# Performance work log

Hardware: AMD Instinct MI355X
Metric: run time of the kernel (lower is better)

## Reference

```python
import jax, jax.numpy as jnp
import numpy as np

NTYPES = 2
NATOMS = (512, 512)
N = 1024          # total atoms
NN = 128          # neighbors per type
M = NTYPES * NN   # 256 neighbor slots per atom
D = 25            # last embedding width
FH = 240          # fitting hidden width
B = 8
RMIN, RMAX = 5.8, 6.0


def _embed_mlp(s, W0, b0, W1, b1, W2, b2):
    # DeepMD-style resnet embedding net: 1 -> D -> D -> D, tanh + skip
    h = jnp.tanh(s @ W0 + b0)
    h = h + jnp.tanh(h @ W1 + b1)
    h = h + jnp.tanh(h @ W2 + b2)
    return h


def setup_inputs() -> dict:
    key = jax.random.key(0)
    ks = jax.random.split(key, 20)
    # relative positions; components in [-4.5, 4.5] so |r| spans <5.8, [5.8,6.0), >=6.0
    image_dR = (jax.random.uniform(ks[0], (B, N, NTYPES, NN, 3), jnp.float32) - 0.5) * 9.0
    # 0 == empty neighbor slot (mask = list_neigh > 0); index-1 in [0, N)
    list_neigh = jax.random.randint(ks[1], (B, N, NTYPES, NN), 0, 1025)
    davg = 0.1 * jax.random.normal(ks[2], (NTYPES, M, 4), jnp.float32)
    dstd = jax.random.uniform(ks[3], (NTYPES, M, 4), jnp.float32, 0.5, 1.5)
    P = NTYPES * NTYPES
    eW0 = jax.random.normal(ks[4], (P, 1, D), jnp.float32)
    eb0 = 0.1 * jax.random.normal(ks[5], (P, D), jnp.float32)
    eW1 = jax.random.normal(ks[6], (P, D, D), jnp.float32) / np.sqrt(D)
    eb1 = 0.1 * jax.random.normal(ks[7], (P, D), jnp.float32)
    eW2 = jax.random.normal(ks[8], (P, D, D), jnp.float32) / np.sqrt(D)
    eb2 = 0.1 * jax.random.normal(ks[9], (P, D), jnp.float32)
    fW0 = jax.random.normal(ks[10], (NTYPES, 16 * D, FH), jnp.float32) / np.sqrt(16 * D)
    fb0 = 0.1 * jax.random.normal(ks[11], (NTYPES, FH), jnp.float32)
    fW1 = jax.random.normal(ks[12], (NTYPES, FH, FH), jnp.float32) / np.sqrt(FH)
    fb1 = 0.1 * jax.random.normal(ks[13], (NTYPES, FH), jnp.float32)
    fW2 = jax.random.normal(ks[14], (NTYPES, FH, FH), jnp.float32) / np.sqrt(FH)
    fb2 = 0.1 * jax.random.normal(ks[15], (NTYPES, FH), jnp.float32)
    fW3 = jax.random.normal(ks[16], (NTYPES, FH, 1), jnp.float32) / np.sqrt(FH)
    fb3 = 0.1 * jax.random.normal(ks[17], (NTYPES, 1), jnp.float32)
    ener_shift = 0.01 * jax.random.normal(ks[18], (NTYPES,), jnp.float32)
    return {
        'image_dR': image_dR, 'list_neigh': list_neigh,
        'davg': davg, 'dstd': dstd,
        'eW0': eW0, 'eb0': eb0, 'eW1': eW1, 'eb1': eb1, 'eW2': eW2, 'eb2': eb2,
        'fW0': fW0, 'fb0': fb0, 'fW1': fW1, 'fb1': fb1, 'fW2': fW2, 'fb2': fb2,
        'fW3': fW3, 'fb3': fb3, 'ener_shift': ener_shift,
        'dfeat': jnp.zeros((1,), jnp.float32),
        'Egroup_weight': jnp.zeros((1,), jnp.float32),
        'divider': jnp.ones((1,), jnp.float32),
    }


def _forward(image_dR, list_neigh, davg, dstd,
             eW0, eb0, eW1, eb1, eW2, eb2,
             fW0, fb0, fW1, fb1, fW2, fb2, fW3, fb3, ener_shift):
    dR = image_dR.reshape(B, N, M, 3)
    neigh = list_neigh.reshape(B, N, M)
    mask = neigh > 0
    mf = mask.astype(dR.dtype)
    dR2 = jnp.sum(dR * dR, axis=-1)                       # [B,N,M]
    safe_dR2 = jnp.where(mask, dR2, 1.0)
    Rij = jnp.sqrt(safe_dR2)
    inr = mf / Rij                                        # 1/|r|, 0 off-mask
    x = Rij * mf                                          # nr = dR2/Rij = |r|
    Ri_xyz = dR / safe_dR2[..., None] * mf[..., None]     # r / |r|^2
    inr2 = inr * inr
    inr4 = inr2 * inr2
    inr3 = inr4 * x
    # smooth switching function on [RMIN, RMAX]
    u = (x - RMIN) / (RMAX - RMIN)
    poly = u * u * u * (-6.0 * u * u + 15.0 * u - 10.0) + 1.0
    dpoly = (3.0 * u * u * (-6.0 * u * u + 15.0 * u - 10.0)
             + u * u * u * (-12.0 * u + 15.0)) / (RMAX - RMIN)
    mid = (x >= RMIN) & (x < RMAX)
    vv = jnp.where(x < RMIN, 1.0, jnp.where(mid, poly, 0.0)) * mf
    dvv = jnp.where(mid, dpoly, 0.0) * mf
    Ri_pre = jnp.concatenate([inr[..., None], Ri_xyz], axis=-1)   # [B,N,M,4]
    common = (dvv * inr)[..., None] * dR                          # [B,N,M,3]
    row0 = dR * (inr3 * vv)[..., None] - Ri_pre[..., 0:1] * common
    eye = jnp.eye(3, dtype=dR.dtype)
    outer = (2.0 * dR[..., :, None] * dR[..., None, :] * inr4[..., None, None]
             - eye * inr2[..., None, None])                       # [B,N,M,3,3]
    rows = outer * vv[..., None, None] - Ri_pre[..., 1:4, None] * common[..., None, :]
    Ri_d = jnp.concatenate([row0[..., None, :], rows], axis=-2) * mf[..., None, None]  # [B,N,M,4,3]
    Ri = Ri_pre * vv[..., None]
    # per-type normalization stats broadcast over atoms of each type
    davg_res = jnp.concatenate([jnp.broadcast_to(davg[t], (NATOMS[t], M, 4)) for t in range(NTYPES)], axis=0)
    dstd_res = jnp.concatenate([jnp.broadcast_to(dstd[t], (NATOMS[t], M, 4)) for t in range(NTYPES)], axis=0)
    Ri = (Ri - davg_res) / dstd_res
    Ri_d = Ri_d / dstd_res[..., None]

    def ei_fn(Ri_n):
        Ei_list = []
        start = 0
        for t in range(NTYPES):
            na = NATOMS[t]
            Rt = jax.lax.slice_in_dim(Ri_n, start, start + na, axis=1)  # [B,na,M,4]
            acc = jnp.zeros((B, na, 4, D), Ri_n.dtype)
            for t1 in range(NTYPES):
                p = t * NTYPES + t1
                blk = Rt[:, :, t1 * NN:(t1 + 1) * NN]                  # [B,na,NN,4]
                G = _embed_mlp(blk[..., 0:1], eW0[p], eb0[p], eW1[p], eb1[p], eW2[p], eb2[p])
                acc = acc + jnp.einsum('bnkd,bnke->bnde', blk, G)
            acc = acc * (4.0 / (NN * NTYPES * 4))
            DRt = jnp.einsum('bnde,bndf->bnef', acc, acc[..., :16]).reshape(B, na, D * 16)
            h = jnp.tanh(DRt @ fW0[t] + fb0[t])
            h = h + jnp.tanh(h @ fW1[t] + fb1[t])
            h = h + jnp.tanh(h @ fW2[t] + fb2[t])
            Ei_list.append(h @ fW3[t] + fb3[t] + ener_shift[t])
            start += na
        return jnp.concatenate(Ei_list, axis=1)   # [B,N,1]

    Ei, vjpf = jax.vjp(ei_fn, Ri)
    dE, = vjpf(jnp.ones_like(Ei))                 # dEi/dRi  [B,N,M,4]
    Etot = jnp.sum(Ei, axis=1)                    # [B,1]
    pair = jnp.einsum('bnmd,bnmdx->bnmx', dE, Ri_d)   # per-pair force term [B,N,M,3]
    F_self = -jnp.sum(pair, axis=2)
    j = neigh - 1
    valid = j >= 0
    flat_idx = jnp.where(valid, j, N) + jnp.arange(B)[:, None, None] * (N + 1)
    contrib = jnp.where(valid[..., None], pair, 0.0)
    seg = jax.ops.segment_sum(contrib.reshape(-1, 3), flat_idx.reshape(-1), num_segments=B * (N + 1))
    F = F_self + seg.reshape(B, N + 1, 3)[:, :N]
    return Etot, Ei, F


def reference(image_dR, list_neigh, davg, dstd,
              eW0, eb0, eW1, eb1, eW2, eb2,
              fW0, fb0, fW1, fb1, fW2, fb2, fW3, fb3, ener_shift,
              dfeat, Egroup_weight, divider):
    # dfeat / Egroup_weight / divider are in the torch forward signature but unused
    return _forward(image_dR, list_neigh, davg, dstd,
                    eW0, eb0, eW1, eb1, eW2, eb2,
                    fW0, fb0, fW1, fb1, fW2, fb2, fW3, fb3, ener_shift)
```

## Files before the change

kernel.cpp:

```cpp
#include <hip/hip_runtime.h>

#define DEV __device__ __forceinline__

namespace {

constexpr int B_ = 8;
constexpr int N_ = 1024;
constexpr int M_ = 256;
constexpr int D_ = 25;
constexpr int FH_ = 240;
constexpr int NATOM = B_ * N_;
constexpr float CSC = 1.0f / 256.0f;

DEV float fast_tanh(float x) {
  float ax = fabsf(x);
  float e = __expf(-2.0f * ax);
  float r = (1.0f - e) * __builtin_amdgcn_rcpf(1.0f + e);
  return copysignf(r, x);
}

struct Geom {
  float mf, inr, inr2, inr4, inr3, vv, dvv;
};

DEV Geom geom_core(float dx, float dy, float dz, int nb) {
  Geom g;
  g.mf = (nb > 0) ? 1.0f : 0.0f;
  float dr2 = dx * dx + dy * dy + dz * dz;
  float safe = (nb > 0) ? dr2 : 1.0f;
  float rs = __builtin_amdgcn_rsqf(safe);
  float rij = safe * rs;
  g.inr = g.mf * rs;
  float x = rij * g.mf;
  g.inr2 = g.inr * g.inr;
  g.inr4 = g.inr2 * g.inr2;
  g.inr3 = g.inr4 * x;
  float u = (x - 5.8f) * 5.0f;
  float uu = u * u;
  float A = -6.0f * uu + 15.0f * u - 10.0f;
  float poly = uu * u * A + 1.0f;
  float dpoly = (3.0f * uu * A + uu * u * (-12.0f * u + 15.0f)) * 5.0f;
  bool mid = (x >= 5.8f) && (x < 6.0f);
  g.vv = ((x < 5.8f) ? 1.0f : (mid ? poly : 0.0f)) * g.mf;
  g.dvv = (mid ? dpoly : 0.0f) * g.mf;
  return g;
}

DEV void geom_blk(const Geom& g, float dx, float dy, float dz, int t, int m,
                  const float* __restrict__ davg, const float* __restrict__ dstd,
                  float* __restrict__ blk, float* __restrict__ rsv) {
  int bidx = (t * M_ + m) * 4;
  float4 av = *(const float4*)(davg + bidx);
  float4 sv = *(const float4*)(dstd + bidx);
  float pre[4] = {g.inr, dx * g.inr2, dy * g.inr2, dz * g.inr2};
  float avf[4] = {av.x, av.y, av.z, av.w};
  float svf[4] = {sv.x, sv.y, sv.z, sv.w};
#pragma unroll
  for (int d = 0; d < 4; ++d) {
    rsv[d] = __builtin_amdgcn_rcpf(svf[d]);
    blk[d] = (pre[d] * g.vv - avf[d]) * rsv[d];
  }
}

__global__ __launch_bounds__(256) void k_embed_acc(
    const float* __restrict__ dR, const int* __restrict__ neigh,
    const float* __restrict__ davg, const float* __restrict__ dstd,
    const float* __restrict__ eW0, const float* __restrict__ eb0,
    const float* __restrict__ eW1, const float* __restrict__ eb1,
    const float* __restrict__ eW2, const float* __restrict__ eb2,
    float* __restrict__ acc_ws) {
  __shared__ float sG[M_ * D_];
  __shared__ float4 sBlk[M_];
  int atom = blockIdx.x;
  int n = atom & (N_ - 1);
  int t = (n >= 512) ? 1 : 0;
  int m = threadIdx.x;
  int p = __builtin_amdgcn_readfirstlane(t * 2 + (m >> 7));
  const float* W0 = eW0 + p * D_;
  const float* b0 = eb0 + p * D_;
  const float* W1 = eW1 + p * D_ * D_;
  const float* b1 = eb1 + p * D_;
  const float* W2 = eW2 + p * D_ * D_;
  const float* b2 = eb2 + p * D_;
  int base = atom * M_ + m;
  float dx = dR[base * 3 + 0];
  float dy = dR[base * 3 + 1];
  float dz = dR[base * 3 + 2];
  int nb = neigh[base];
  Geom g = geom_core(dx, dy, dz, nb);
  float blk[4], rsv[4];
  geom_blk(g, dx, dy, dz, t, m, davg, dstd, blk, rsv);
  float s = blk[0];
  float h[D_], a[D_];
#pragma unroll
  for (int e = 0; e < D_; ++e) h[e] = fast_tanh(fmaf(s, W0[e], b0[e]));
#pragma unroll
  for (int e = 0; e < D_; ++e) a[e] = b1[e];
#pragma unroll
  for (int f = 0; f < D_; ++f) {
    float hf = h[f];
#pragma unroll
    for (int e = 0; e < D_; ++e) a[e] = fmaf(hf, W1[f * D_ + e], a[e]);
  }
#pragma unroll
  for (int e = 0; e < D_; ++e) h[e] += fast_tanh(a[e]);
#pragma unroll
  for (int e = 0; e < D_; ++e) a[e] = b2[e];
#pragma unroll
  for (int f = 0; f < D_; ++f) {
    float hf = h[f];
#pragma unroll
    for (int e = 0; e < D_; ++e) a[e] = fmaf(hf, W2[f * D_ + e], a[e]);
  }
#pragma unroll
  for (int e = 0; e < D_; ++e) sG[m * D_ + e] = h[e] + fast_tanh(a[e]);
  sBlk[m] = make_float4(blk[0], blk[1], blk[2], blk[3]);
  __syncthreads();
  if (threadIdx.x < 100) {
    int d = threadIdx.x & 3;
    int e = threadIdx.x >> 2;
    const float* sb = (const float*)sBlk;
    float s0 = 0.0f, s1 = 0.0f, s2 = 0.0f, s3 = 0.0f;
    for (int mm = 0; mm < M_; mm += 4) {
      s0 = fmaf(sb[(mm + 0) * 4 + d], sG[(mm + 0) * D_ + e], s0);
      s1 = fmaf(sb[(mm + 1) * 4 + d], sG[(mm + 1) * D_ + e], s1);
      s2 = fmaf(sb[(mm + 2) * 4 + d], sG[(mm + 2) * D_ + e], s2);
      s3 = fmaf(sb[(mm + 3) * 4 + d], sG[(mm + 3) * D_ + e], s3);
    }
    acc_ws[atom * 100 + d * D_ + e] = ((s0 + s1) + (s2 + s3)) * CSC;
  }
}

__global__ __launch_bounds__(256) void k_fit(
    const float* __restrict__ acc_ws,
    const float* __restrict__ fW0, const float* __restrict__ fb0,
    const float* __restrict__ fW1, const float* __restrict__ fb1,
    const float* __restrict__ fW2, const float* __restrict__ fb2,
    const float* __restrict__ fW3, const float* __restrict__ fb3,
    const float* __restrict__ ener_shift,
    float* __restrict__ dacc_ws, float* __restrict__ out) {
  constexpr int AB = 8;
  __shared__ float sAcc[AB][100];
  __shared__ float sX[AB][400];
  __shared__ float sH0[AB][FH_];
  __shared__ float sT1[AB][FH_];
  __shared__ float sH1[AB][FH_];
  __shared__ float sT2[AB][FH_];
  __shared__ float sEi[AB];
  int a0 = blockIdx.x * AB;
  int bb = a0 >> 10;
  int n0 = a0 & (N_ - 1);
  int t = (n0 >= 512) ? 1 : 0;
  int tid = threadIdx.x;
  for (int idx = tid; idx < AB * 100; idx += 256)
    ((float*)sAcc)[idx] = acc_ws[a0 * 100 + idx];
  if (tid < AB) sEi[tid] = 0.0f;
  __syncthreads();
  for (int idx = tid; idx < AB * 400; idx += 256) {
    int a = idx / 400; int r = idx % 400; int e = r >> 4; int f = r & 15;
    const float* A = sAcc[a];
    sX[a][r] = A[e] * A[f] + A[25 + e] * A[25 + f] + A[50 + e] * A[50 + f] +
               A[75 + e] * A[75 + f];
  }
  __syncthreads();
  const float* W0 = fW0 + t * 400 * FH_;
  const float* W1 = fW1 + t * FH_ * FH_;
  const float* W2 = fW2 + t * FH_ * FH_;
  const float* B0 = fb0 + t * FH_;
  const float* B1 = fb1 + t * FH_;
  const float* B2 = fb2 + t * FH_;
  const float* W3 = fW3 + t * FH_;
  int j = tid;
  if (j < FH_) {
    float acc8[AB];
#pragma unroll
    for (int a = 0; a < AB; ++a) acc8[a] = B0[j];
    for (int i = 0; i < 400; ++i) {
      float w = W0[i * FH_ + j];
#pragma unroll
      for (int a = 0; a < AB; ++a) acc8[a] = fmaf(sX[a][i], w, acc8[a]);
    }
#pragma unroll
    for (int a = 0; a < AB; ++a) sH0[a][j] = fast_tanh(acc8[a]);
  }
  __syncthreads();
  if (j < FH_) {
    float acc8[AB];
#pragma unroll
    for (int a = 0; a < AB; ++a) acc8[a] = B1[j];
    for (int f = 0; f < FH_; ++f) {
      float w = W1[f * FH_ + j];
#pragma unroll
      for (int a = 0; a < AB; ++a) acc8[a] = fmaf(sH0[a][f], w, acc8[a]);
    }
#pragma unroll
    for (int a = 0; a < AB; ++a) {
      float tv = fast_tanh(acc8[a]);
      sT1[a][j] = tv;
      sH1[a][j] = sH0[a][j] + tv;
    }
  }
  __syncthreads();
  if (j < FH_) {
    float acc8[AB];
#pragma unroll
    for (int a = 0; a < AB; ++a) acc8[a] = B2[j];
    for (int f = 0; f < FH_; ++f) {
      float w = W2[f * FH_ + j];
#pragma unroll
      for (int a = 0; a < AB; ++a) acc8[a] = fmaf(sH1[a][f], w, acc8[a]);
    }
    float w3 = W3[j];
#pragma unroll
    for (int a = 0; a < AB; ++a) {
      float tv = fast_tanh(acc8[a]);
      sT2[a][j] = tv;
      atomicAdd(&sEi[a], (sH1[a][j] + tv) * w3);
    }
  }
  __syncthreads();
  if (tid < AB) {
    float ei = sEi[tid] + fb3[t] + ener_shift[t];
    out[8 + a0 + tid] = ei;
    atomicAdd(&out[bb], ei);
  }
  if (j < FH_) {
    float w3 = W3[j];
#pragma unroll
    for (int a = 0; a < AB; ++a) {
      float tv = sT2[a][j];
      sT2[a][j] = w3 * (1.0f - tv * tv);
    }
  }
  __syncthreads();
  if (j < FH_) {
    float w3 = W3[j];
    float acc8[AB];
#pragma unroll
    for (int a = 0; a < AB; ++a) acc8[a] = w3;
    for (int k = 0; k < FH_; ++k) {
      float w = W2[j * FH_ + k];
#pragma unroll
      for (int a = 0; a < AB; ++a) acc8[a] = fmaf(sT2[a][k], w, acc8[a]);
    }
#pragma unroll
    for (int a = 0; a < AB; ++a) {
      float dh1 = acc8[a];
      float tv = sT1[a][j];
      sH1[a][j] = dh1;
      sT1[a][j] = dh1 * (1.0f - tv * tv);
    }
  }
  __syncthreads();
  if (j < FH_) {
    float acc8[AB];
#pragma unroll
    for (int a = 0; a < AB; ++a) acc8[a] = sH1[a][j];
    for (int k = 0; k < FH_; ++k) {
      float w = W1[j * FH_ + k];
#pragma unroll
      for (int a = 0; a < AB; ++a) acc8[a] = fmaf(sT1[a][k], w, acc8[a]);
    }
#pragma unroll
    for (int a = 0; a < AB; ++a) {
      float h0v = sH0[a][j];
      sH0[a][j] = acc8[a] * (1.0f - h0v * h0v);
    }
  }
  __syncthreads();
  for (int i = tid; i < 400; i += 256) {
    float acc8[AB];
#pragma unroll
    for (int a = 0; a < AB; ++a) acc8[a] = 0.0f;
    for (int jj = 0; jj < FH_; ++jj) {
      float w = W0[i * FH_ + jj];
#pragma unroll
      for (int a = 0; a < AB; ++a) acc8[a] = fmaf(sH0[a][jj], w, acc8[a]);
    }
#pragma unroll
    for (int a = 0; a < AB; ++a) sX[a][i] = acc8[a];
  }
  __syncthreads();
  for (int idx = tid; idx < AB * 100; idx += 256) {
    int a = idx / 100; int r = idx % 100; int d = r / 25; int e = r % 25;
    const float* A = sAcc[a];
    const float* DX = sX[a];
    float sum = 0.0f;
#pragma unroll
    for (int f = 0; f < 16; ++f) sum = fmaf(DX[e * 16 + f], A[d * 25 + f], sum);
    if (e < 16) {
#pragma unroll
      for (int e2 = 0; e2 < 25; ++e2) sum = fmaf(DX[e2 * 16 + e], A[d * 25 + e2], sum);
    }
    dacc_ws[a0 * 100 + idx] = sum;
  }
}

__global__ __launch_bounds__(256) __attribute__((amdgpu_waves_per_eu(4)))
void k_bwd_force(
    const float* __restrict__ dR, const int* __restrict__ neigh,
    const float* __restrict__ davg, const float* __restrict__ dstd,
    const float* __restrict__ eW0, const float* __restrict__ eb0,
    const float* __restrict__ eW1, const float* __restrict__ eb1,
    const float* __restrict__ eW2, const float* __restrict__ eb2,
    const float* __restrict__ dacc_ws, float* __restrict__ out) {
  __shared__ float sHP[D_][256];
  int atom = blockIdx.x;
  int bb = atom >> 10;
  int n = atom & (N_ - 1);
  int t = (n >= 512) ? 1 : 0;
  int m = threadIdx.x;
  int p = __builtin_amdgcn_readfirstlane(t * 2 + (m >> 7));
  const float* W0 = eW0 + p * D_;
  const float* b0 = eb0 + p * D_;
  const float* W1 = eW1 + p * D_ * D_;
  const float* b1 = eb1 + p * D_;
  const float* W2 = eW2 + p * D_ * D_;
  const float* b2 = eb2 + p * D_;
  const float* dac = dacc_ws + atom * 100;
  int base = atom * M_ + m;
  float dx = dR[base * 3 + 0];
  float dy = dR[base * 3 + 1];
  float dz = dR[base * 3 + 2];
  int nb = neigh[base];
  Geom g = geom_core(dx, dy, dz, nb);
  float blk[4], rsv[4];
  geom_blk(g, dx, dy, dz, t, m, davg, dstd, blk, rsv);

  float s = blk[0];
  float h[D_];
#pragma unroll
  for (int e = 0; e < D_; ++e) {
    float th = fast_tanh(fmaf(s, W0[e], b0[e]));
    h[e] = th;
    sHP[e][m] = (1.0f - th * th) * W0[e];
  }
  {
    float a[D_], ap[D_];
#pragma unroll
    for (int e = 0; e < D_; ++e) { a[e] = b1[e]; ap[e] = 0.0f; }
#pragma unroll
    for (int f = 0; f < D_; ++f) {
      float hf = h[f];
      float hpf = sHP[f][m];
#pragma unroll
      for (int e = 0; e < D_; ++e) {
        float w = W1[f * D_ + e];
        a[e] = fmaf(hf, w, a[e]);
        ap[e] = fmaf(hpf, w, ap[e]);
      }
    }
#pragma unroll
    for (int e = 0; e < D_; ++e) {
      float th = fast_tanh(a[e]);
      sHP[e][m] = fmaf(1.0f - th * th, ap[e], sHP[e][m]);
      h[e] += th;
    }
  }
  float ds = 0.0f, db0 = 0.0f, db1 = 0.0f, db2 = 0.0f, db3 = 0.0f;
  {
    float a[D_], ap[D_];
#pragma unroll
    for (int e = 0; e < D_; ++e) { a[e] = b2[e]; ap[e] = 0.0f; }
#pragma unroll
    for (int f = 0; f < D_; ++f) {
      float hf = h[f];
      float hpf = sHP[f][m];
#pragma unroll
      for (int e = 0; e < D_; ++e) {
        float w = W2[f * D_ + e];
        a[e] = fmaf(hf, w, a[e]);
        ap[e] = fmaf(hpf, w, ap[e]);
      }
    }
#pragma unroll
    for (int e = 0; e < D_; ++e) {
      float th = fast_tanh(a[e]);
      float G = h[e] + th;
      float hp2 = fmaf(1.0f - th * th, ap[e], sHP[e][m]);
      float d0 = dac[e], d1 = dac[25 + e], d2 = dac[50 + e], d3 = dac[75 + e];
      float u = d0 * blk[0] + d1 * blk[1] + d2 * blk[2] + d3 * blk[3];
      ds = fmaf(u, hp2, ds);
      db0 = fmaf(d0, G, db0);
      db1 = fmaf(d1, G, db1);
      db2 = fmaf(d2, G, db2);
      db3 = fmaf(d3, G, db3);
    }
  }
  float dE0 = (db0 + ds) * CSC;
  float dE1 = db1 * CSC, dE2 = db2 * CSC, dE3 = db3 * CSC;

  float dv[3] = {dx, dy, dz};
  float pre1[3] = {dx * g.inr2, dy * g.inr2, dz * g.inr2};
  float ci = g.dvv * g.inr;
  float com[3];
#pragma unroll
  for (int c = 0; c < 3; ++c) com[c] = ci * dv[c];
  float iv = g.inr3 * g.vv;
  float pc[3];
  float f0 = dE0 * rsv[0];
#pragma unroll
  for (int c = 0; c < 3; ++c) pc[c] = f0 * (dv[c] * iv - g.inr * com[c]);
  float dEr[3] = {dE1, dE2, dE3};
#pragma unroll
  for (int r = 0; r < 3; ++r) {
    float fr = dEr[r] * rsv[1 + r];
#pragma unroll
    for (int c = 0; c < 3; ++c) {
      float outer = 2.0f * dv[r] * dv[c] * g.inr4 - ((r == c) ? g.inr2 : 0.0f);
      pc[c] = fmaf(fr, outer * g.vv - pre1[r] * com[c], pc[c]);
    }
  }
  float px = pc[0] * g.mf, py = pc[1] * g.mf, pz = pc[2] * g.mf;

  if (nb > 0) {
    int jn = nb - 1;
    int fi = 8 + NATOM + (bb * N_ + jn) * 3;
    atomicAdd(&out[fi + 0], px);
    atomicAdd(&out[fi + 1], py);
    atomicAdd(&out[fi + 2], pz);
  }
#pragma unroll
  for (int i = 1; i < 64; i <<= 1) {
    px += __shfl_xor(px, i);
    py += __shfl_xor(py, i);
    pz += __shfl_xor(pz, i);
  }
  if ((m & 63) == 0) {
    int fi = 8 + NATOM + atom * 3;
    atomicAdd(&out[fi + 0], -px);
    atomicAdd(&out[fi + 1], -py);
    atomicAdd(&out[fi + 2], -pz);
  }
}

}

extern "C" void kernel_launch(void* const* d_in, const int* in_sizes, int n_in,
                              void* d_out, int out_size, void* d_ws, size_t ws_size,
                              hipStream_t stream) {
  (void)in_sizes; (void)n_in; (void)ws_size;
  const float* image_dR   = (const float*)d_in[0];
  const int*   list_neigh = (const int*)d_in[1];
  const float* davg       = (const float*)d_in[2];
  const float* dstd       = (const float*)d_in[3];
  const float* eW0        = (const float*)d_in[4];
  const float* eb0        = (const float*)d_in[5];
  const float* eW1        = (const float*)d_in[6];
  const float* eb1        = (const float*)d_in[7];
  const float* eW2        = (const float*)d_in[8];
  const float* eb2        = (const float*)d_in[9];
  const float* fW0        = (const float*)d_in[10];
  const float* fb0        = (const float*)d_in[11];
  const float* fW1        = (const float*)d_in[12];
  const float* fb1        = (const float*)d_in[13];
  const float* fW2        = (const float*)d_in[14];
  const float* fb2        = (const float*)d_in[15];
  const float* fW3        = (const float*)d_in[16];
  const float* fb3        = (const float*)d_in[17];
  const float* ener_shift = (const float*)d_in[18];
  float* out = (float*)d_out;
  float* acc_ws  = (float*)d_ws;
  float* dacc_ws = acc_ws + NATOM * 100;

  hipMemsetAsync(d_out, 0, (size_t)out_size * sizeof(float), stream);
  k_embed_acc<<<NATOM, 256, 0, stream>>>(image_dR, list_neigh, davg, dstd,
                                         eW0, eb0, eW1, eb1, eW2, eb2, acc_ws);
  k_fit<<<NATOM / 8, 256, 0, stream>>>(acc_ws, fW0, fb0, fW1, fb1, fW2, fb2,
                                       fW3, fb3, ener_shift, dacc_ws, out);
  k_bwd_force<<<NATOM, 256, 0, stream>>>(image_dR, list_neigh, davg, dstd,
                                         eW0, eb0, eW1, eb1, eW2, eb2,
                                         dacc_ws, out);
}
```

Measured before the change: 986.4 us.

## Stage embedding weights in LDS and restructure embedding loops to cut register pressure

Both embedding kernels now copy the per-type embedding weights and biases into padded shared-memory rows at block start. Weight rows are read as float4 vectors inside non-unrolled loops, replacing the fully unrolled global/scalar weight loads. The backward kernel drops its sHP shared scratch, keeps hidden derivatives in registers, and walks the second layer by output column using a transposed W2. The intent is to lower register pressure and instruction count so occupancy rises. The cost is an extra staging phase and barrier per block, and the tanh of layer 0 is computed twice.

```diff
diff --git a/kernel.cpp b/kernel.cpp
--- a/kernel.cpp
+++ b/kernel.cpp
@@ -11,6 +11,8 @@
 constexpr int FH_ = 240;
 constexpr int NATOM = B_ * N_;
 constexpr float CSC = 1.0f / 256.0f;
+constexpr int WROW = 28;
+constexpr int WSZ = 100 + 2 * D_ * WROW;
 
 DEV float fast_tanh(float x) {
   float ax = fabsf(x);
@@ -62,6 +64,46 @@
   }
 }
 
+DEV void load_wrow(const float* __restrict__ wr, float* __restrict__ wrow) {
+#pragma unroll
+  for (int k = 0; k < 7; ++k) {
+    float4 qv = ((const float4*)wr)[k];
+    wrow[4 * k + 0] = qv.x;
+    wrow[4 * k + 1] = qv.y;
+    wrow[4 * k + 2] = qv.z;
+    wrow[4 * k + 3] = qv.w;
+  }
+}
+
+template <bool TRANSPOSE_W2>
+DEV void stage_weights(int tid, int t,
+                       const float* __restrict__ eW0, const float* __restrict__ eb0,
+                       const float* __restrict__ eW1, const float* __restrict__ eb1,
+                       const float* __restrict__ eW2, const float* __restrict__ eb2,
+                       float* __restrict__ sW) {
+  for (int idx = tid; idx < 2 * WSZ; idx += 256) {
+    int pl = idx / WSZ;
+    int r = idx - pl * WSZ;
+    int pp = t * 2 + pl;
+    float v = 0.0f;
+    if (r < 25) v = eW0[pp * 25 + r];
+    else if (r < 50) v = eb0[pp * 25 + r - 25];
+    else if (r < 75) v = eb1[pp * 25 + r - 50];
+    else if (r < 100) v = eb2[pp * 25 + r - 75];
+    else if (r < 100 + D_ * WROW) {
+      int rr = r - 100;
+      int f = rr / WROW, e = rr - f * WROW;
+      if (e < 25) v = eW1[pp * 625 + f * 25 + e];
+    } else {
+      int rr = r - (100 + D_ * WROW);
+      int i = rr / WROW, j = rr - i * WROW;
+      if (j < 25) v = TRANSPOSE_W2 ? eW2[pp * 625 + j * 25 + i]
+                                   : eW2[pp * 625 + i * 25 + j];
+    }
+    sW[idx] = v;
+  }
+}
+
 __global__ __launch_bounds__(256) void k_embed_acc(
     const float* __restrict__ dR, const int* __restrict__ neigh,
     const float* __restrict__ davg, const float* __restrict__ dstd,
@@ -71,17 +113,15 @@
     float* __restrict__ acc_ws) {
   __shared__ float sG[M_ * D_];
   __shared__ float4 sBlk[M_];
+  __shared__ __align__(16) float sW[2 * WSZ];
   int atom = blockIdx.x;
   int n = atom & (N_ - 1);
   int t = (n >= 512) ? 1 : 0;
   int m = threadIdx.x;
-  int p = __builtin_amdgcn_readfirstlane(t * 2 + (m >> 7));
-  const float* W0 = eW0 + p * D_;
-  const float* b0 = eb0 + p * D_;
-  const float* W1 = eW1 + p * D_ * D_;
-  const float* b1 = eb1 + p * D_;
-  const float* W2 = eW2 + p * D_ * D_;
-  const float* b2 = eb2 + p * D_;
+  stage_weights<false>(m, t, eW0, eb0, eW1, eb1, eW2, eb2, sW);
+  __syncthreads();
+  int pl = __builtin_amdgcn_readfirstlane(m >> 7);
+  const float* wp = sW + pl * WSZ;
   int base = atom * M_ + m;
   float dx = dR[base * 3 + 0];
   float dy = dR[base * 3 + 1];
@@ -90,31 +130,40 @@
   Geom g = geom_core(dx, dy, dz, nb);
   float blk[4], rsv[4];
   geom_blk(g, dx, dy, dz, t, m, davg, dstd, blk, rsv);
+  sBlk[m] = make_float4(blk[0], blk[1], blk[2], blk[3]);
   float s = blk[0];
-  float h[D_], a[D_];
-#pragma unroll
-  for (int e = 0; e < D_; ++e) h[e] = fast_tanh(fmaf(s, W0[e], b0[e]));
-#pragma unroll
-  for (int e = 0; e < D_; ++e) a[e] = b1[e];
-#pragma unroll
+  float* hcol = sG + m * D_;
+  float a[D_];
+#pragma unroll
+  for (int e = 0; e < D_; ++e) a[e] = wp[50 + e];
+#pragma unroll 1
   for (int f = 0; f < D_; ++f) {
-    float hf = h[f];
-#pragma unroll
-    for (int e = 0; e < D_; ++e) a[e] = fmaf(hf, W1[f * D_ + e], a[e]);
-  }
-#pragma unroll
-  for (int e = 0; e < D_; ++e) h[e] += fast_tanh(a[e]);
-#pragma unroll
-  for (int e = 0; e < D_; ++e) a[e] = b2[e];
-#pragma unroll
+    float th0 = fast_tanh(fmaf(s, wp[f], wp[25 + f]));
+    float wrow[WROW];
+    load_wrow(wp + 100 + f * WROW, wrow);
+#pragma unroll
+    for (int e = 0; e < D_; ++e) a[e] = fmaf(th0, wrow[e], a[e]);
+  }
+  float h1r[D_];
+#pragma unroll
+  for (int e = 0; e < D_; ++e) {
+    float th0 = fast_tanh(fmaf(s, wp[e], wp[25 + e]));
+    h1r[e] = th0 + fast_tanh(a[e]);
+    hcol[e] = h1r[e];
+  }
+  float a2[D_];
+#pragma unroll
+  for (int e = 0; e < D_; ++e) a2[e] = wp[75 + e];
+#pragma unroll 1
   for (int f = 0; f < D_; ++f) {
-    float hf = h[f];
-#pragma unroll
-    for (int e = 0; e < D_; ++e) a[e] = fmaf(hf, W2[f * D_ + e], a[e]);
-  }
-#pragma unroll
-  for (int e = 0; e < D_; ++e) sG[m * D_ + e] = h[e] + fast_tanh(a[e]);
-  sBlk[m] = make_float4(blk[0], blk[1], blk[2], blk[3]);
+    float hf = hcol[f];
+    float wrow[WROW];
+    load_wrow(wp + 100 + D_ * WROW + f * WROW, wrow);
+#pragma unroll
+    for (int e = 0; e < D_; ++e) a2[e] = fmaf(hf, wrow[e], a2[e]);
+  }
+#pragma unroll
+  for (int e = 0; e < D_; ++e) hcol[e] = h1r[e] + fast_tanh(a2[e]);
   __syncthreads();
   if (threadIdx.x < 100) {
     int d = threadIdx.x & 3;
@@ -296,7 +345,7 @@
   }
 }
 
-__global__ __launch_bounds__(256) __attribute__((amdgpu_waves_per_eu(4)))
+__global__ __launch_bounds__(256) __attribute__((amdgpu_waves_per_eu(4, 4)))
 void k_bwd_force(
     const float* __restrict__ dR, const int* __restrict__ neigh,
     const float* __restrict__ davg, const float* __restrict__ dstd,
@@ -304,19 +353,16 @@
     const float* __restrict__ eW1, const float* __restrict__ eb1,
     const float* __restrict__ eW2, const float* __restrict__ eb2,
     const float* __restrict__ dacc_ws, float* __restrict__ out) {
-  __shared__ float sHP[D_][256];
+  __shared__ __align__(16) float sW[2 * WSZ];
   int atom = blockIdx.x;
   int bb = atom >> 10;
   int n = atom & (N_ - 1);
   int t = (n >= 512) ? 1 : 0;
   int m = threadIdx.x;
-  int p = __builtin_amdgcn_readfirstlane(t * 2 + (m >> 7));
-  const float* W0 = eW0 + p * D_;
-  const float* b0 = eb0 + p * D_;
-  const float* W1 = eW1 + p * D_ * D_;
-  const float* b1 = eb1 + p * D_;
-  const float* W2 = eW2 + p * D_ * D_;
-  const float* b2 = eb2 + p * D_;
+  stage_weights<true>(m, t, eW0, eb0, eW1, eb1, eW2, eb2, sW);
+  __syncthreads();
+  int pl = __builtin_amdgcn_readfirstlane(m >> 7);
+  const float* wp = sW + pl * WSZ;
   const float* dac = dacc_ws + atom * 100;
   int base = atom * M_ + m;
   float dx = dR[base * 3 + 0];
@@ -326,66 +372,65 @@
   Geom g = geom_core(dx, dy, dz, nb);
   float blk[4], rsv[4];
   geom_blk(g, dx, dy, dz, t, m, davg, dstd, blk, rsv);
-
   float s = blk[0];
-  float h[D_];
+
+  float a[D_], ap[D_];
+#pragma unroll
+  for (int e = 0; e < D_; ++e) { a[e] = wp[50 + e]; ap[e] = 0.0f; }
+#pragma unroll 1
+  for (int f = 0; f < D_; ++f) {
+    float w0f = wp[f];
+    float th0 = fast_tanh(fmaf(s, w0f, wp[25 + f]));
+    float hp0 = (1.0f - th0 * th0) * w0f;
+    float wrow[WROW];
+    load_wrow(wp + 100 + f * WROW, wrow);
+#pragma unroll
+    for (int e = 0; e < D_; ++e) {
+      a[e] = fmaf(th0, wrow[e], a[e]);
+      ap[e] = fmaf(hp0, wrow[e], ap[e]);
+    }
+  }
+  float h1[D_], hp1[D_];
 #pragma unroll
   for (int e = 0; e < D_; ++e) {
-    float th = fast_tanh(fmaf(s, W0[e], b0[e]));
-    h[e] = th;
-    sHP[e][m] = (1.0f - th * th) * W0[e];
-  }
-  {
-    float a[D_], ap[D_];
-#pragma unroll
-    for (int e = 0; e < D_; ++e) { a[e] = b1[e]; ap[e] = 0.0f; }
+    float w0e = wp[e];
+    float th0 = fast_tanh(fmaf(s, w0e, wp[25 + e]));
+    float hp0 = (1.0f - th0 * th0) * w0e;
+    float th1 = fast_tanh(a[e]);
+    h1[e] = th0 + th1;
+    hp1[e] = fmaf(1.0f - th1 * th1, ap[e], hp0);
+  }
+
+  float ds = 0.0f, db0 = 0.0f, db1 = 0.0f, db2 = 0.0f, db3 = 0.0f;
+#pragma unroll
+  for (int e = 0; e < D_; ++e) {
+    float d0 = dac[e], d1 = dac[25 + e], d2 = dac[50 + e], d3 = dac[75 + e];
+    float he = h1[e];
+    db0 = fmaf(d0, he, db0);
+    db1 = fmaf(d1, he, db1);
+    db2 = fmaf(d2, he, db2);
+    db3 = fmaf(d3, he, db3);
+    float u = d0 * blk[0] + d1 * blk[1] + d2 * blk[2] + d3 * blk[3];
+    ds = fmaf(u, hp1[e], ds);
+  }
+#pragma unroll 1
+  for (int e = 0; e < D_; ++e) {
+    float wrow[WROW];
+    load_wrow(wp + 100 + D_ * WROW + e * WROW, wrow);
+    float a2 = wp[75 + e], ap2 = 0.0f;
 #pragma unroll
     for (int f = 0; f < D_; ++f) {
-      float hf = h[f];
-      float hpf = sHP[f][m];
-#pragma unroll
-      for (int e = 0; e < D_; ++e) {
-        float w = W1[f * D_ + e];
-        a[e] = fmaf(hf, w, a[e]);
-        ap[e] = fmaf(hpf, w, ap[e]);
-      }
-    }
-#pragma unroll
-    for (int e = 0; e < D_; ++e) {
-      float th = fast_tanh(a[e]);
-      sHP[e][m] = fmaf(1.0f - th * th, ap[e], sHP[e][m]);
-      h[e] += th;
-    }
-  }
-  float ds = 0.0f, db0 = 0.0f, db1 = 0.0f, db2 = 0.0f, db3 = 0.0f;
-  {
-    float a[D_], ap[D_];
-#pragma unroll
-    for (int e = 0; e < D_; ++e) { a[e] = b2[e]; ap[e] = 0.0f; }
-#pragma unroll
-    for (int f = 0; f < D_; ++f) {
-      float hf = h[f];
-      float hpf = sHP[f][m];
-#pragma unroll
-      for (int e = 0; e < D_; ++e) {
-        float w = W2[f * D_ + e];
-        a[e] = fmaf(hf, w, a[e]);
-        ap[e] = fmaf(hpf, w, ap[e]);
-      }
-    }
-#pragma unroll
-    for (int e = 0; e < D_; ++e) {
-      float th = fast_tanh(a[e]);
-      float G = h[e] + th;
-      float hp2 = fmaf(1.0f - th * th, ap[e], sHP[e][m]);
-      float d0 = dac[e], d1 = dac[25 + e], d2 = dac[50 + e], d3 = dac[75 + e];
-      float u = d0 * blk[0] + d1 * blk[1] + d2 * blk[2] + d3 * blk[3];
-      ds = fmaf(u, hp2, ds);
-      db0 = fmaf(d0, G, db0);
-      db1 = fmaf(d1, G, db1);
-      db2 = fmaf(d2, G, db2);
-      db3 = fmaf(d3, G, db3);
-    }
+      a2 = fmaf(h1[f], wrow[f], a2);
+      ap2 = fmaf(hp1[f], wrow[f], ap2);
+    }
+    float th = fast_tanh(a2);
+    float d0 = dac[e], d1 = dac[25 + e], d2 = dac[50 + e], d3 = dac[75 + e];
+    db0 = fmaf(d0, th, db0);
+    db1 = fmaf(d1, th, db1);
+    db2 = fmaf(d2, th, db2);
+    db3 = fmaf(d3, th, db3);
+    float u = d0 * blk[0] + d1 * blk[1] + d2 * blk[2] + d3 * blk[3];
+    ds = fmaf(u, (1.0f - th * th) * ap2, ds);
   }
   float dE0 = (db0 + ds) * CSC;
   float dE1 = db1 * CSC, dE2 = db2 * CSC, dE3 = db3 * CSC;
```

Result: slower. 1.030 ms (+4.4%).

## Accumulate forces in shared memory per atom group and reduce partials

Applied to the files above, without the earlier changes.

The backward force kernel now has each block handle 16 atoms of one batch sample and scatter neighbor forces into a shared-memory force array with LDS atomics, instead of issuing global atomics per pair. Each block writes its full per-sample partial force array to workspace, and a new reduction kernel sums the 64 partials per sample into the output. This removes heavy global atomic contention, at the cost of 512 blocks instead of 8192 (less parallelism and occupancy), 12KB extra LDS per block, and about 12MB of partial writes and reads. The waves_per_eu attribute was also dropped.

```diff
diff --git a/kernel.cpp b/kernel.cpp
--- a/kernel.cpp
+++ b/kernel.cpp
@@ -11,6 +11,8 @@
 constexpr int FH_ = 240;
 constexpr int NATOM = B_ * N_;
 constexpr float CSC = 1.0f / 256.0f;
+constexpr int GATOMS = 16;
+constexpr int GROUPS = N_ / GATOMS;
 
 DEV float fast_tanh(float x) {
   float ax = fabsf(x);
@@ -296,20 +298,22 @@
   }
 }
 
-__global__ __launch_bounds__(256) __attribute__((amdgpu_waves_per_eu(4)))
-void k_bwd_force(
+__global__ __launch_bounds__(256) void k_bwd_force(
     const float* __restrict__ dR, const int* __restrict__ neigh,
     const float* __restrict__ davg, const float* __restrict__ dstd,
     const float* __restrict__ eW0, const float* __restrict__ eb0,
     const float* __restrict__ eW1, const float* __restrict__ eb1,
     const float* __restrict__ eW2, const float* __restrict__ eb2,
-    const float* __restrict__ dacc_ws, float* __restrict__ out) {
+    const float* __restrict__ dacc_ws, float* __restrict__ partials) {
   __shared__ float sHP[D_][256];
-  int atom = blockIdx.x;
-  int bb = atom >> 10;
-  int n = atom & (N_ - 1);
-  int t = (n >= 512) ? 1 : 0;
+  __shared__ float sF[N_ * 3];
+  int bg = blockIdx.x;
+  int b = bg / GROUPS;
+  int grp = bg - b * GROUPS;
+  int n0 = grp * GATOMS;
+  int t = (n0 >= 512) ? 1 : 0;
   int m = threadIdx.x;
+  for (int i = m; i < N_ * 3; i += 256) sF[i] = 0.0f;
   int p = __builtin_amdgcn_readfirstlane(t * 2 + (m >> 7));
   const float* W0 = eW0 + p * D_;
   const float* b0 = eb0 + p * D_;
@@ -317,121 +321,145 @@
   const float* b1 = eb1 + p * D_;
   const float* W2 = eW2 + p * D_ * D_;
   const float* b2 = eb2 + p * D_;
-  const float* dac = dacc_ws + atom * 100;
-  int base = atom * M_ + m;
-  float dx = dR[base * 3 + 0];
-  float dy = dR[base * 3 + 1];
-  float dz = dR[base * 3 + 2];
-  int nb = neigh[base];
-  Geom g = geom_core(dx, dy, dz, nb);
-  float blk[4], rsv[4];
-  geom_blk(g, dx, dy, dz, t, m, davg, dstd, blk, rsv);
-
-  float s = blk[0];
-  float h[D_];
-#pragma unroll
-  for (int e = 0; e < D_; ++e) {
-    float th = fast_tanh(fmaf(s, W0[e], b0[e]));
-    h[e] = th;
-    sHP[e][m] = (1.0f - th * th) * W0[e];
-  }
-  {
-    float a[D_], ap[D_];
-#pragma unroll
-    for (int e = 0; e < D_; ++e) { a[e] = b1[e]; ap[e] = 0.0f; }
-#pragma unroll
-    for (int f = 0; f < D_; ++f) {
-      float hf = h[f];
-      float hpf = sHP[f][m];
+  __syncthreads();
+
+#pragma unroll 1
+  for (int k = 0; k < GATOMS; ++k) {
+    int n = n0 + k;
+    int atom = b * N_ + n;
+    const float* dac = dacc_ws + atom * 100;
+    int base = atom * M_ + m;
+    float dx = dR[base * 3 + 0];
+    float dy = dR[base * 3 + 1];
+    float dz = dR[base * 3 + 2];
+    int nb = neigh[base];
+    Geom g = geom_core(dx, dy, dz, nb);
+    float blk[4], rsv[4];
+    geom_blk(g, dx, dy, dz, t, m, davg, dstd, blk, rsv);
+    float s = blk[0];
+
+    float h[D_];
+#pragma unroll
+    for (int e = 0; e < D_; ++e) {
+      float th = fast_tanh(fmaf(s, W0[e], b0[e]));
+      h[e] = th;
+      sHP[e][m] = (1.0f - th * th) * W0[e];
+    }
+    {
+      float a[D_], ap[D_];
+#pragma unroll
+      for (int e = 0; e < D_; ++e) { a[e] = b1[e]; ap[e] = 0.0f; }
+#pragma unroll
+      for (int f = 0; f < D_; ++f) {
+        float hf = h[f];
+        float hpf = sHP[f][m];
+#pragma unroll
+        for (int e = 0; e < D_; ++e) {
+          float w = W1[f * D_ + e];
+          a[e] = fmaf(hf, w, a[e]);
+          ap[e] = fmaf(hpf, w, ap[e]);
+        }
+      }
 #pragma unroll
       for (int e = 0; e < D_; ++e) {
-        float w = W1[f * D_ + e];
-        a[e] = fmaf(hf, w, a[e]);
-        ap[e] = fmaf(hpf, w, ap[e]);
+        float th = fast_tanh(a[e]);
+        sHP[e][m] = fmaf(1.0f - th * th, ap[e], sHP[e][m]);
+        h[e] += th;
       }
     }
-#pragma unroll
-    for (int e = 0; e < D_; ++e) {
-      float th = fast_tanh(a[e]);
-      sHP[e][m] = fmaf(1.0f - th * th, ap[e], sHP[e][m]);
-      h[e] += th;
-    }
-  }
-  float ds = 0.0f, db0 = 0.0f, db1 = 0.0f, db2 = 0.0f, db3 = 0.0f;
-  {
-    float a[D_], ap[D_];
-#pragma unroll
-    for (int e = 0; e < D_; ++e) { a[e] = b2[e]; ap[e] = 0.0f; }
-#pragma unroll
-    for (int f = 0; f < D_; ++f) {
-      float hf = h[f];
-      float hpf = sHP[f][m];
+    float ds = 0.0f, db0 = 0.0f, db1 = 0.0f, db2 = 0.0f, db3 = 0.0f;
+    {
+      float a[D_], ap[D_];
+#pragma unroll
+      for (int e = 0; e < D_; ++e) { a[e] = b2[e]; ap[e] = 0.0f; }
+#pragma unroll
+      for (int f = 0; f < D_; ++f) {
+        float hf = h[f];
+        float hpf = sHP[f][m];
+#pragma unroll
+        for (int e = 0; e < D_; ++e) {
+          float w = W2[f * D_ + e];
+          a[e] = fmaf(hf, w, a[e]);
+          ap[e] = fmaf(hpf, w, ap[e]);
+        }
+      }
 #pragma unroll
       for (int e = 0; e < D_; ++e) {
-        float w = W2[f * D_ + e];
-        a[e] = fmaf(hf, w, a[e]);
-        ap[e] = fmaf(hpf, w, ap[e]);
+        float th = fast_tanh(a[e]);
+        float G = h[e] + th;
+        float hp2 = fmaf(1.0f - th * th, ap[e], sHP[e][m]);
+        float d0 = dac[e], d1 = dac[25 + e], d2 = dac[50 + e], d3 = dac[75 + e];
+        float u = d0 * blk[0] + d1 * blk[1] + d2 * blk[2] + d3 * blk[3];
+        ds = fmaf(u, hp2, ds);
+        db0 = fmaf(d0, G, db0);
+        db1 = fmaf(d1, G, db1);
+        db2 = fmaf(d2, G, db2);
+        db3 = fmaf(d3, G, db3);
       }
     }
-#pragma unroll
-    for (int e = 0; e < D_; ++e) {
-      float th = fast_tanh(a[e]);
-      float G = h[e] + th;
-      float hp2 = fmaf(1.0f - th * th, ap[e], sHP[e][m]);
-      float d0 = dac[e], d1 = dac[25 + e], d2 = dac[50 + e], d3 = dac[75 + e];
-      float u = d0 * blk[0] + d1 * blk[1] + d2 * blk[2] + d3 * blk[3];
-      ds = fmaf(u, hp2, ds);
-      db0 = fmaf(d0, G, db0);
-      db1 = fmaf(d1, G, db1);
-      db2 = fmaf(d2, G, db2);
-      db3 = fmaf(d3, G, db3);
-    }
-  }
-  float dE0 = (db0 + ds) * CSC;
-  float dE1 = db1 * CSC, dE2 = db2 * CSC, dE3 = db3 * CSC;
-
-  float dv[3] = {dx, dy, dz};
-  float pre1[3] = {dx * g.inr2, dy * g.inr2, dz * g.inr2};
-  float ci = g.dvv * g.inr;
-  float com[3];
-#pragma unroll
-  for (int c = 0; c < 3; ++c) com[c] = ci * dv[c];
-  float iv = g.inr3 * g.vv;
-  float pc[3];
-  float f0 = dE0 * rsv[0];
-#pragma unroll
-  for (int c = 0; c < 3; ++c) pc[c] = f0 * (dv[c] * iv - g.inr * com[c]);
-  float dEr[3] = {dE1, dE2, dE3};
-#pragma unroll
-  for (int r = 0; r < 3; ++r) {
-    float fr = dEr[r] * rsv[1 + r];
-#pragma unroll
-    for (int c = 0; c < 3; ++c) {
-      float outer = 2.0f * dv[r] * dv[c] * g.inr4 - ((r == c) ? g.inr2 : 0.0f);
-      pc[c] = fmaf(fr, outer * g.vv - pre1[r] * com[c], pc[c]);
-    }
-  }
-  float px = pc[0] * g.mf, py = pc[1] * g.mf, pz = pc[2] * g.mf;
-
-  if (nb > 0) {
-    int jn = nb - 1;
-    int fi = 8 + NATOM + (bb * N_ + jn) * 3;
-    atomicAdd(&out[fi + 0], px);
-    atomicAdd(&out[fi + 1], py);
-    atomicAdd(&out[fi + 2], pz);
-  }
-#pragma unroll
-  for (int i = 1; i < 64; i <<= 1) {
-    px += __shfl_xor(px, i);
-    py += __shfl_xor(py, i);
-    pz += __shfl_xor(pz, i);
-  }
-  if ((m & 63) == 0) {
-    int fi = 8 + NATOM + atom * 3;
-    atomicAdd(&out[fi + 0], -px);
-    atomicAdd(&out[fi + 1], -py);
-    atomicAdd(&out[fi + 2], -pz);
-  }
+    float dE0 = (db0 + ds) * CSC;
+    float dE1 = db1 * CSC, dE2 = db2 * CSC, dE3 = db3 * CSC;
+
+    float dv[3] = {dx, dy, dz};
+    float pre1[3] = {dx * g.inr2, dy * g.inr2, dz * g.inr2};
+    float ci = g.dvv * g.inr;
+    float com[3];
+#pragma unroll
+    for (int c = 0; c < 3; ++c) com[c] = ci * dv[c];
+    float iv = g.inr3 * g.vv;
+    float pc[3];
+    float f0 = dE0 * rsv[0];
+#pragma unroll
+    for (int c = 0; c < 3; ++c) pc[c] = f0 * (dv[c] * iv - g.inr * com[c]);
+    float dEr[3] = {dE1, dE2, dE3};
+#pragma unroll
+    for (int r = 0; r < 3; ++r) {
+      float fr = dEr[r] * rsv[1 + r];
+#pragma unroll
+      for (int c = 0; c < 3; ++c) {
+        float outer = 2.0f * dv[r] * dv[c] * g.inr4 - ((r == c) ? g.inr2 : 0.0f);
+        pc[c] = fmaf(fr, outer * g.vv - pre1[r] * com[c], pc[c]);
+      }
+    }
+    float px = pc[0] * g.mf, py = pc[1] * g.mf, pz = pc[2] * g.mf;
+
+    if (nb > 0) {
+      int jn = nb - 1;
+      atomicAdd(&sF[jn * 3 + 0], px);
+      atomicAdd(&sF[jn * 3 + 1], py);
+      atomicAdd(&sF[jn * 3 + 2], pz);
+    }
+#pragma unroll
+    for (int i = 1; i < 64; i <<= 1) {
+      px += __shfl_xor(px, i);
+      py += __shfl_xor(py, i);
+      pz += __shfl_xor(pz, i);
+    }
+    if ((m & 63) == 0) {
+      atomicAdd(&sF[n * 3 + 0], -px);
+      atomicAdd(&sF[n * 3 + 1], -py);
+      atomicAdd(&sF[n * 3 + 2], -pz);
+    }
+  }
+  __syncthreads();
+  float* pb = partials + (size_t)bg * (N_ * 3);
+  for (int i = m; i < N_ * 3; i += 256) pb[i] = sF[i];
+}
+
+__global__ __launch_bounds__(256) void k_freduce(
+    const float* __restrict__ partials, float* __restrict__ out) {
+  int idx = blockIdx.x * 256 + threadIdx.x;
+  int b = idx / (N_ * 3);
+  int r = idx - b * (N_ * 3);
+  const float* pp = partials + (size_t)(b * GROUPS) * (N_ * 3) + r;
+  float s0 = 0.0f, s1 = 0.0f, s2 = 0.0f, s3 = 0.0f;
+  for (int g = 0; g < GROUPS; g += 4) {
+    s0 += pp[(g + 0) * (N_ * 3)];
+    s1 += pp[(g + 1) * (N_ * 3)];
+    s2 += pp[(g + 2) * (N_ * 3)];
+    s3 += pp[(g + 3) * (N_ * 3)];
+  }
+  out[8 + NATOM + idx] = (s0 + s1) + (s2 + s3);
 }
 
 }
@@ -460,15 +488,17 @@
   const float* fb3        = (const float*)d_in[17];
   const float* ener_shift = (const float*)d_in[18];
   float* out = (float*)d_out;
-  float* acc_ws  = (float*)d_ws;
-  float* dacc_ws = acc_ws + NATOM * 100;
+  float* acc_ws   = (float*)d_ws;
+  float* dacc_ws  = acc_ws + NATOM * 100;
+  float* partials = dacc_ws + NATOM * 100;
 
   hipMemsetAsync(d_out, 0, (size_t)out_size * sizeof(float), stream);
   k_embed_acc<<<NATOM, 256, 0, stream>>>(image_dR, list_neigh, davg, dstd,
                                          eW0, eb0, eW1, eb1, eW2, eb2, acc_ws);
   k_fit<<<NATOM / 8, 256, 0, stream>>>(acc_ws, fW0, fb0, fW1, fb1, fW2, fb2,
                                        fW3, fb3, ener_shift, dacc_ws, out);
-  k_bwd_force<<<NATOM, 256, 0, stream>>>(image_dR, list_neigh, davg, dstd,
-                                         eW0, eb0, eW1, eb1, eW2, eb2,
-                                         dacc_ws, out);
-}
+  k_bwd_force<<<B_ * GROUPS, 256, 0, stream>>>(image_dR, list_neigh, davg, dstd,
+                                               eW0, eb0, eW1, eb1, eW2, eb2,
+                                               dacc_ws, partials);
+  k_freduce<<<(B_ * N_ * 3) / 256, 256, 0, stream>>>(partials, out);
+}
```

New measurement: 1.010 ms. +2.4%, slower.
